# Kernel optimization log

Hardware: AMD Instinct MI355X
Metric: run time of the kernel (lower is better)

## Reference

```python
import jax, jax.numpy as jnp
from jax import lax
import numpy as np

B, C_IN, IMG = 32, 4, 224
FH = FW = IMG // 8  # 28: three stride-2 maxpools
NA = 4
SCORE_T, IOU_T, MAXP = 0.7, 0.3, 10
EPS = 1e-5


def conv2d(x, w, b, pad):
    y = lax.conv_general_dilated(x, w, (1, 1), [(pad, pad), (pad, pad)],
                                 dimension_numbers=('NCHW', 'OIHW', 'NCHW'))
    return y + b[None, :, None, None]


def bn_eval(x, g, b):
    # eval-mode BN with running_mean=0, running_var=1 (fresh model), eps=1e-5
    return x * (g / jnp.sqrt(1.0 + EPS))[None, :, None, None] + b[None, :, None, None]


def maxpool2(x):
    return lax.reduce_window(x, -jnp.inf, lax.max, (1, 1, 2, 2), (1, 1, 2, 2), 'VALID')


def make_anchors():
    ys = (jnp.arange(FH) + 0.5) / FH
    xs = (jnp.arange(FW) + 0.5) / FW
    cy, cx = jnp.meshgrid(ys, xs, indexing='ij')
    cxy = jnp.stack([cx, cy], -1)  # [H,W,2], matches loop order y,x then anchor
    sizes = jnp.array([[16., 16.], [32., 32.], [64., 64.], [128., 128.]], jnp.float32) / 224.0
    a = jnp.concatenate([jnp.broadcast_to(cxy[:, :, None, :], (FH, FW, NA, 2)),
                         jnp.broadcast_to(sizes[None, None], (FH, FW, NA, 2))], -1)
    return a.reshape(-1, 4)  # [H*W*NA, 4] = [3136, 4]


def decode_boxes(anchors, offsets):
    centers = anchors[..., :2] + offsets[..., :2] * 0.1
    sizes = anchors[..., 2:] * jnp.exp(offsets[..., 2:] * 0.2)
    boxes = jnp.concatenate([centers - sizes / 2, centers + sizes / 2], -1)
    return jnp.clip(boxes, 0.0, 1.0)


def nms_single(boxes, scores):
    # greedy NMS, fixed MAXP iterations (== max_proposals_per_image cap)
    N = scores.shape[0]
    s0 = jnp.where(scores > SCORE_T, scores, -jnp.inf)  # score-threshold filter
    areas = (boxes[:, 2] - boxes[:, 0]) * (boxes[:, 3] - boxes[:, 1])
    idx_all = jnp.arange(N)

    def body(s, _):
        i = jnp.argmax(s)
        ok = s[i] > -jnp.inf
        bi = boxes[i]
        xx1 = jnp.maximum(bi[0], boxes[:, 0]); yy1 = jnp.maximum(bi[1], boxes[:, 1])
        xx2 = jnp.minimum(bi[2], boxes[:, 2]); yy2 = jnp.minimum(bi[3], boxes[:, 3])
        inter = jnp.clip(xx2 - xx1, 0.0) * jnp.clip(yy2 - yy1, 0.0)
        iou = inter / (areas[i] + areas - inter)
        sup = (iou > IOU_T) | (idx_all == i)
        s_next = jnp.where(ok & sup, -jnp.inf, s)
        return s_next, (jnp.where(ok, i, 0), ok)

    _, (idxs, oks) = lax.scan(body, s0, None, length=MAXP)
    return idxs, oks  # [MAXP] int32, [MAXP] bool


def _forward(x, r1w, r1b, g1, b1, r2w, r2b, g2, b2, r3w, r3b, g3, b3, rpw, rpb,
             clsw, clsb, regw, regb, c1w, c1b, cg1, cb1, c2w, c2b, cg2, cb2,
             fc1w, fc1b, fc2w, fc2b, fc3w, fc3b, fc4w, fc4b):
    Bsz = x.shape[0]
    # --- Stage 1: lightweight RPN ---
    h = maxpool2(jax.nn.relu(bn_eval(conv2d(x, r1w, r1b, 1), g1, b1)))
    h = maxpool2(jax.nn.relu(bn_eval(conv2d(h, r2w, r2b, 1), g2, b2)))
    h = maxpool2(jax.nn.relu(bn_eval(conv2d(h, r3w, r3b, 1), g3, b3)))
    h = jax.nn.relu(conv2d(h, rpw, rpb, 1))
    cls = conv2d(h, clsw, clsb, 0).transpose(0, 2, 3, 1).reshape(Bsz, -1, 2)
    reg = conv2d(h, regw, regb, 0).transpose(0, 2, 3, 1).reshape(Bsz, -1, 4)
    anchors = make_anchors()
    probs = jax.nn.softmax(cls, -1)[..., 1]        # [B,N] objectness
    boxes = decode_boxes(anchors[None], reg)       # [B,N,4]
    # --- proposal selection: score threshold + greedy NMS + top-10 cap ---
    idxs, oks = jax.vmap(nms_single)(boxes, probs)  # [B,10]
    okf = oks.astype(boxes.dtype)
    kept_boxes = jax.vmap(lambda b, i: b[i])(boxes, idxs) * okf[..., None]
    kept_scores = jax.vmap(lambda s, i: s[i])(probs, idxs) * okf
    has_prop = (probs > SCORE_T).any(-1)           # [B]
    # --- Stage 2: CLM classifier (applied to the full image, as in original) ---
    f = jax.nn.relu(bn_eval(conv2d(x, c1w, c1b, 1), cg1, cb1))
    f = jax.nn.relu(bn_eval(conv2d(f, c2w, c2b, 1), cg2, cb2))
    # AdaptiveAvgPool2d((7,7)) on 224x224 -> mean over 32x32 blocks
    f = f.reshape(Bsz, 128, 7, 32, 7, 32).mean(axis=(3, 5)).reshape(Bsz, -1)
    f = jax.nn.relu(f @ fc1w + fc1b)
    f = jax.nn.relu(f @ fc2w + fc2b)
    f = jax.nn.relu(f @ fc3w + fc3b)
    logits = f @ fc4w + fc4b
    bg = jnp.array([1.0, 0.0], logits.dtype)
    final = jnp.where(has_prop[:, None], logits, bg[None])
    return final, kept_boxes, kept_scores, oks


def setup_inputs() -> dict:
    key = jax.random.key(0)
    ks = iter(jax.random.split(key, 64))

    def conv_w(o, i, k):
        return jax.random.normal(next(ks), (o, i, k, k), jnp.float32) * float(np.sqrt(2.0 / (i * k * k)))

    def lin_w(i, o):
        return jax.random.normal(next(ks), (i, o), jnp.float32) * float(1.0 / np.sqrt(i))

    return {
        'x': jax.random.normal(next(ks), (B, C_IN, IMG, IMG), jnp.float32),
        'r1w': conv_w(32, 4, 3), 'r1b': jnp.zeros(32), 'g1': jnp.ones(32), 'b1': jnp.zeros(32),
        'r2w': conv_w(64, 32, 3), 'r2b': jnp.zeros(64), 'g2': jnp.ones(64), 'b2': jnp.zeros(64),
        'r3w': conv_w(128, 64, 3), 'r3b': jnp.zeros(128), 'g3': jnp.ones(128), 'b3': jnp.zeros(128),
        'rpw': conv_w(256, 128, 3), 'rpb': jnp.zeros(256),
        'clsw': conv_w(8, 256, 1), 'clsb': jnp.zeros(8),
        'regw': conv_w(16, 256, 1), 'regb': jnp.zeros(16),
        'c1w': conv_w(64, 4, 3), 'c1b': jnp.zeros(64), 'cg1': jnp.ones(64), 'cb1': jnp.zeros(64),
        'c2w': conv_w(128, 64, 3), 'c2b': jnp.zeros(128), 'cg2': jnp.ones(128), 'cb2': jnp.zeros(128),
        'fc1w': lin_w(6272, 512), 'fc1b': jnp.zeros(512),
        'fc2w': lin_w(512, 256), 'fc2b': jnp.zeros(256),
        'fc3w': lin_w(256, 128), 'fc3b': jnp.zeros(128),
        'fc4w': lin_w(128, 2), 'fc4b': jnp.zeros(2),
    }


def reference(x, r1w, r1b, g1, b1, r2w, r2b, g2, b2, r3w, r3b, g3, b3, rpw, rpb,
              clsw, clsb, regw, regb, c1w, c1b, cg1, cb1, c2w, c2b, cg2, cb2,
              fc1w, fc1b, fc2w, fc2b, fc3w, fc3b, fc4w, fc4b):
    return _forward(x, r1w, r1b, g1, b1, r2w, r2b, g2, b2, r3w, r3b, g3, b3, rpw, rpb,
                    clsw, clsb, regw, regb, c1w, c1b, cg1, cb1, c2w, c2b, cg2, cb2,
                    fc1w, fc1b, fc2w, fc2b, fc3w, fc3b, fc4w, fc4b)
```

## Files before the change

### kernel.cpp

```cpp
#include <hip/hip_runtime.h>
#include <math.h>

constexpr int NANCH = 3136;
constexpr float SCORE_T = 0.7f;
constexpr float IOU_T = 0.3f;
constexpr int MAXP = 10;

typedef unsigned short u16;
typedef __attribute__((ext_vector_type(8))) short short8x;
typedef __attribute__((ext_vector_type(4))) float f32x4;

__device__ inline u16 f2bf(float f) {
  unsigned u = __builtin_bit_cast(unsigned, f);
  u += 0x7fffu + ((u >> 16) & 1u);
  return (u16)(u >> 16);
}
__device__ inline float bf2f(u16 h) {
  unsigned u = ((unsigned)h) << 16;
  return __builtin_bit_cast(float, u);
}

__global__ __launch_bounds__(256) void w1prep_k(const float* __restrict__ w,
                                                u16* __restrict__ hi, u16* __restrict__ lo,
                                                int COUT) {
  const int i = blockIdx.x * 256 + threadIdx.x;
  if (i >= COUT * 64) return;
  const int k = i & 63, co = i >> 6;
  float v = 0.f;
  if (k < 36) { const int tap = k >> 2, cin = k & 3; v = w[co * 36 + cin * 9 + tap]; }
  const u16 h = f2bf(v);
  hi[i] = h;
  lo[i] = f2bf(v - bf2f(h));
}

template<int MODE>
__global__ __launch_bounds__(256) void c1mfma_k(
    const float* __restrict__ x,
    const u16* __restrict__ wfh, const u16* __restrict__ wfl,
    const float* __restrict__ bias, const float* __restrict__ gamma,
    const float* __restrict__ beta,
    u16* __restrict__ outhi, u16* __restrict__ outlo) {
  constexpr int COUT = MODE ? 32 : 64;
  constexpr int NF   = MODE ? 2 : 4;
  constexpr int PS   = MODE ? 136 : 72;
  __shared__ u16 s_patch[64 * PS];
  __shared__ u16 s_wh[COUT * 72];
  __shared__ u16 s_wl[MODE ? COUT * 72 : 8];
  __shared__ float s_raw[4 * 6 * 18];
  __shared__ float s_pool[MODE ? 4 * 16 * 17 : 1];
  __shared__ u16 s_out[MODE ? 8 : 64 * 72];

  const int tid = threadIdx.x, lane = tid & 63, w = tid >> 6;
  const int lr = lane & 15, lg = lane >> 4;
  const int img = blockIdx.z;
  const int x0 = blockIdx.x * 16, y0 = blockIdx.y * 4;

  for (int i = tid; i < 64 * 7; i += 256) {
    const int p = i / 7, q = i % 7;
    *(uint2*)&s_patch[p * PS + 36 + q * 4] = make_uint2(0, 0);
    if (MODE) *(uint2*)&s_patch[p * PS + 100 + q * 4] = make_uint2(0, 0);
  }
  for (int i = tid; i < 432; i += 256) {
    const int cin = i / 108, r = i % 108;
    const int ry = r / 18, rx = r % 18;
    const int gy = y0 - 1 + ry, gx = x0 - 1 + rx;
    float v = 0.f;
    if ((unsigned)gy < 224u && (unsigned)gx < 224u)
      v = x[(((size_t)img * 4 + cin) * 224 + gy) * 224 + gx];
    s_raw[i] = v;
  }
  for (int i = tid; i < COUT * 8; i += 256) {
    const int co = i >> 3, q = i & 7;
    *(uint4*)&s_wh[co * 72 + q * 8] = *(const uint4*)&wfh[co * 64 + q * 8];
    if (MODE) *(uint4*)&s_wl[co * 72 + q * 8] = *(const uint4*)&wfl[co * 64 + q * 8];
  }
  __syncthreads();

  for (int i = tid; i < 576; i += 256) {
    const int p = i / 9, tap = i % 9;
    const int ty = p >> 4, tx = p & 15;
    const int ky = tap / 3, kx = tap % 3;
    u16 h4[4], l4[4];
#pragma unroll
    for (int cin = 0; cin < 4; cin++) {
      const float v = s_raw[cin * 108 + (ty + ky) * 18 + (tx + kx)];
      h4[cin] = f2bf(v);
      if (MODE) l4[cin] = f2bf(v - bf2f(h4[cin]));
    }
    *(uint2*)&s_patch[p * PS + tap * 4] = *(uint2*)h4;
    if (MODE) *(uint2*)&s_patch[p * PS + 64 + tap * 4] = *(uint2*)l4;
  }
  __syncthreads();

  int pA;
  if (MODE) pA = ((w >> 1) * 2 + (lr >> 3)) * 16 + (w & 1) * 8 + (lr & 7);
  else      pA = w * 16 + lr;

  f32x4 acc[NF];
#pragma unroll
  for (int nf = 0; nf < NF; nf++) acc[nf] = (f32x4)(0.f);

#pragma unroll
  for (int ks = 0; ks < 2; ks++) {
    const short8x ah = *(const short8x*)&s_patch[pA * PS + ks * 32 + lg * 8];
    short8x al;
    if (MODE) al = *(const short8x*)&s_patch[pA * PS + 64 + ks * 32 + lg * 8];
#pragma unroll
    for (int nf = 0; nf < NF; nf++) {
      const short8x bh = *(const short8x*)&s_wh[(nf * 16 + lr) * 72 + ks * 32 + lg * 8];
      if (MODE) {
        const short8x bl = *(const short8x*)&s_wl[(nf * 16 + lr) * 72 + ks * 32 + lg * 8];
        acc[nf] = __builtin_amdgcn_mfma_f32_16x16x32_bf16(al, bh, acc[nf], 0, 0, 0);
        acc[nf] = __builtin_amdgcn_mfma_f32_16x16x32_bf16(ah, bl, acc[nf], 0, 0, 0);
      }
      acc[nf] = __builtin_amdgcn_mfma_f32_16x16x32_bf16(ah, bh, acc[nf], 0, 0, 0);
    }
  }

  const float rsq = 1.f / sqrtf(1.f + 1e-5f);

  if (MODE == 0) {
#pragma unroll
    for (int nf = 0; nf < 4; nf++) {
      const int co = nf * 16 + lr;
      const float bi = bias[co], scl = gamma[co] * rsq, shf = beta[co];
#pragma unroll
      for (int j = 0; j < 4; j++) {
        const float e = fmaxf((acc[nf][j] + bi) * scl + shf, 0.f);
        s_out[(w * 16 + lg * 4 + j) * 72 + co] = f2bf(e);
      }
    }
    __syncthreads();
    for (int i = tid; i < 512; i += 256) {
      const int p = i >> 3, q = i & 7;
      const int oy = y0 + (p >> 4), ox = x0 + (p & 15);
      *(uint4*)&outhi[(((size_t)img * 224 + oy) * 224 + ox) * 64 + q * 8] =
          *(uint4*)&s_out[p * 72 + q * 8];
    }
  } else {
#pragma unroll
    for (int nf = 0; nf < 2; nf++) {
      const int co = nf * 16 + lr;
      const float bi = bias[co], scl = gamma[co] * rsq, shf = beta[co];
#pragma unroll
      for (int j = 0; j < 4; j++) {
        const int m = lg * 4 + j;
        s_pool[w * 272 + m * 17 + lr] = (acc[nf][j] + bi) * scl + shf;
      }
      __syncthreads();
      {
        const int pc = lane >> 4, n = lane & 15;
        const float* sp = &s_pool[w * 272];
        float m0 = fmaxf(sp[(pc * 2) * 17 + n], sp[(pc * 2 + 1) * 17 + n]);
        float m1 = fmaxf(sp[(pc * 2 + 8) * 17 + n], sp[(pc * 2 + 9) * 17 + n]);
        const float mm = fmaxf(fmaxf(m0, m1), 0.f);
        const int py = (y0 >> 1) + (w >> 1), px = (x0 >> 1) + (w & 1) * 4 + pc;
        const size_t o = (((size_t)img * 112 + py) * 112 + px) * 32 + nf * 16 + n;
        const u16 h = f2bf(mm);
        outhi[o] = h; outlo[o] = f2bf(mm - bf2f(h));
      }
      __syncthreads();
    }
  }
}

__global__ __launch_bounds__(256) void wsplit_k(const float* __restrict__ w,
                                                u16* __restrict__ hi, u16* __restrict__ lo,
                                                int COUT, int CIN) {
  const int n = 9 * COUT * CIN;
  const int i = blockIdx.x * 256 + threadIdx.x;
  if (i >= n) return;
  const int cin = i % CIN; int r = i / CIN;
  const int cout = r % COUT; const int tap = r / COUT;
  const float v = w[((size_t)cout * CIN + cin) * 9 + tap];
  const u16 h = f2bf(v);
  hi[i] = h; lo[i] = f2bf(v - bf2f(h));
}

__global__ __launch_bounds__(256) void w2b_k(const float* __restrict__ w,
                                             u16* __restrict__ wb) {
  const int i = blockIdx.x * 256 + threadIdx.x;
  if (i >= 73728) return;
  const int cin = i & 63; const int r = i >> 6;
  const int cout = r & 127; const int tap = r >> 7;
  wb[i] = f2bf(w[(((size_t)cout * 64 + cin) * 3 + tap / 3) * 3 + tap % 3]);
}

template<int CINCH, bool POOL, bool BN>
__global__ __launch_bounds__(256) void sconv_k(
    const u16* __restrict__ ahi, const u16* __restrict__ alo,
    const u16* __restrict__ whi, const u16* __restrict__ wlo,
    const float* __restrict__ bias, const float* __restrict__ gamma,
    const float* __restrict__ beta,
    u16* __restrict__ ohi, u16* __restrict__ olo, float* __restrict__ of32,
    int H, int W, int COUT, int cog) {
  __shared__ u16 s_in[6 * 34 * 72];
  __shared__ u16 s_w[64 * 72];
  const int tid = threadIdx.x, lane = tid & 63, wave = tid >> 6;
  const int wm = wave >> 1, wn = wave & 1, lr = lane & 15, lg = lane >> 4;
  const int img = blockIdx.z / cog, co0 = (blockIdx.z % cog) * 64;
  const int x0 = blockIdx.x * 32, band = blockIdx.y;
  const int CIN = CINCH * 32;

  f32x4 acc[4][2];
#pragma unroll
  for (int mi = 0; mi < 4; ++mi) { acc[mi][0] = (f32x4)(0.f); acc[mi][1] = (f32x4)(0.f); }

  for (int cc2 = 0; cc2 < CINCH; ++cc2) {
    for (int idx = tid; idx < 1632; idx += 256) {
      const int r = idx / 272, rem = idx % 272;
      const int c = rem >> 3, q = rem & 7, pl = q >> 2, qq = q & 3;
      const int gy = band * 4 - 1 + r, gx = x0 - 1 + c;
      uint4 v = make_uint4(0, 0, 0, 0);
      if ((unsigned)gy < (unsigned)H && (unsigned)gx < (unsigned)W) {
        const u16* src = pl ? alo : ahi;
        v = *(const uint4*)(src + ((size_t)(img * H + gy) * W + gx) * CIN + cc2 * 32 + qq * 8);
      }
      *(uint4*)(&s_in[(r * 34 + c) * 72 + pl * 32 + qq * 8]) = v;
    }
    for (int tap = 0; tap < 9; ++tap) {
      const int ky = tap / 3, kx = tap % 3;
      for (int idx = tid; idx < 512; idx += 256) {
        const int cout = idx >> 3, q = idx & 7, pl = q >> 2, qq = q & 3;
        const u16* src = pl ? wlo : whi;
        uint4 v = *(const uint4*)(src + ((size_t)tap * COUT + co0 + cout) * CIN + cc2 * 32 + qq * 8);
        *(uint4*)(&s_w[cout * 72 + pl * 32 + qq * 8]) = v;
      }
      __syncthreads();
      short8x ah[4], al[4], bh[2], bl[2];
#pragma unroll
      for (int mi = 0; mi < 4; ++mi) {
        const int base = ((2 * wm + (mi >> 1) + ky) * 34 + (mi & 1) * 16 + lr + kx) * 72;
        ah[mi] = *(const short8x*)(&s_in[base + lg * 8]);
        al[mi] = *(const short8x*)(&s_in[base + 32 + lg * 8]);
      }
#pragma unroll
      for (int ni = 0; ni < 2; ++ni) {
        const int wb2 = (wn * 32 + ni * 16 + lr) * 72;
        bh[ni] = *(const short8x*)(&s_w[wb2 + lg * 8]);
        bl[ni] = *(const short8x*)(&s_w[wb2 + 32 + lg * 8]);
      }
#pragma unroll
      for (int mi = 0; mi < 4; ++mi)
#pragma unroll
        for (int ni = 0; ni < 2; ++ni) {
          acc[mi][ni] = __builtin_amdgcn_mfma_f32_16x16x32_bf16(al[mi], bh[ni], acc[mi][ni], 0, 0, 0);
          acc[mi][ni] = __builtin_amdgcn_mfma_f32_16x16x32_bf16(ah[mi], bl[ni], acc[mi][ni], 0, 0, 0);
          acc[mi][ni] = __builtin_amdgcn_mfma_f32_16x16x32_bf16(ah[mi], bh[ni], acc[mi][ni], 0, 0, 0);
        }
      __syncthreads();
    }
  }

  const float rsq = 1.f / sqrtf(1.f + 1e-5f);
#pragma unroll
  for (int ni = 0; ni < 2; ++ni) {
    const int cout = co0 + wn * 32 + ni * 16 + lr;
    const float bi = bias[cout];
    const float scl = BN ? gamma[cout] * rsq : 1.f;
    const float shf = BN ? beta[cout] : 0.f;
    if (POOL) {
      const int OH = H >> 1, OW = W >> 1;
      const int py = band * 2 + wm;
#pragma unroll
      for (int ch = 0; ch < 2; ++ch)
#pragma unroll
        for (int jp = 0; jp < 2; ++jp) {
          float m = (acc[ch][ni][2 * jp] + bi) * scl + shf;
          m = fmaxf(m, (acc[ch][ni][2 * jp + 1] + bi) * scl + shf);
          m = fmaxf(m, (acc[ch + 2][ni][2 * jp] + bi) * scl + shf);
          m = fmaxf(m, (acc[ch + 2][ni][2 * jp + 1] + bi) * scl + shf);
          m = fmaxf(m, 0.f);
          const int px = (x0 >> 1) + ch * 8 + lg * 2 + jp;
          if (px < OW) {
            const size_t o = ((size_t)(img * OH + py) * OW + px) * COUT + cout;
            const u16 h = f2bf(m);
            ohi[o] = h; olo[o] = f2bf(m - bf2f(h));
          }
        }
    } else {
#pragma unroll
      for (int mi = 0; mi < 4; ++mi) {
        const int row = band * 4 + 2 * wm + (mi >> 1);
#pragma unroll
        for (int j = 0; j < 4; ++j) {
          const int px = x0 + (mi & 1) * 16 + lg * 4 + j;
          if (px < W)
            of32[((size_t)(img * H + row) * W + px) * COUT + cout] =
                fmaxf(acc[mi][ni][j] + bi, 0.f);
        }
      }
    }
  }
}

__global__ __launch_bounds__(256) void c2band_k(
    const u16* __restrict__ act, const u16* __restrict__ wb,
    const float* __restrict__ bias, const float* __restrict__ gamma,
    const float* __restrict__ beta, float* __restrict__ pooled, int gimg0) {
  __shared__ u16 s_in[6 * 34 * 72];
  __shared__ u16 s_w[2 * 128 * 40];
  __shared__ float s_pool[128];

  const int tid = threadIdx.x;
  const int lane = tid & 63, wave = tid >> 6;
  const int wm = wave >> 1, wn = wave & 1;
  const int lr = lane & 15, lg = lane >> 4;
  const int img = blockIdx.z >> 3, band = blockIdx.z & 7;
  const int x0 = blockIdx.x * 32, y0 = blockIdx.y * 32;
  const float rsq = 1.f / sqrtf(1.f + 1e-5f);

  if (tid < 128) s_pool[tid] = 0.f;

  for (int idx = tid; idx < 1632; idx += 256) {
    const int r = idx / 272, rem = idx % 272;
    const int c = rem >> 3, q = rem & 7;
    const int gy = y0 + band * 4 - 1 + r, gx = x0 - 1 + c;
    uint4 v = make_uint4(0, 0, 0, 0);
    if ((unsigned)gy < 224u && (unsigned)gx < 224u)
      v = *(const uint4*)(act + (((size_t)img * 224 + gy) * 224 + gx) * 64 + q * 8);
    *(uint4*)(&s_in[(r * 34 + c) * 72 + q * 8]) = v;
  }

  f32x4 acc[4][4];
#pragma unroll
  for (int mi = 0; mi < 4; ++mi)
#pragma unroll
    for (int ni = 0; ni < 4; ++ni) acc[mi][ni] = (f32x4)(0.f);

  for (int tap = 0; tap < 9; ++tap) {
    const int ky = tap / 3, kx = tap % 3;
    for (int idx = tid; idx < 1024; idx += 256) {
      const int cout = idx >> 3, q = idx & 7;
      uint4 v = *(const uint4*)(wb + ((size_t)tap * 128 + cout) * 64 + q * 8);
      *(uint4*)(&s_w[(q >> 2) * 5120 + cout * 40 + (q & 3) * 8]) = v;
    }
    __syncthreads();
#pragma unroll
    for (int h = 0; h < 2; ++h) {
      short8x a[4], bf[4];
#pragma unroll
      for (int mi = 0; mi < 4; ++mi) {
        const int rl = wm * 2 + (mi >> 1) + ky;
        const int cc = (mi & 1) * 16 + lr + kx;
        a[mi] = *(const short8x*)(&s_in[(rl * 34 + cc) * 72 + h * 32 + lg * 8]);
      }
#pragma unroll
      for (int ni = 0; ni < 4; ++ni) {
        const int co = wn * 64 + ni * 16 + lr;
        bf[ni] = *(const short8x*)(&s_w[h * 5120 + co * 40 + lg * 8]);
      }
#pragma unroll
      for (int mi = 0; mi < 4; ++mi)
#pragma unroll
        for (int ni = 0; ni < 4; ++ni)
          acc[mi][ni] = __builtin_amdgcn_mfma_f32_16x16x32_bf16(a[mi], bf[ni], acc[mi][ni], 0, 0, 0);
    }
    __syncthreads();
  }
#pragma unroll
  for (int ni = 0; ni < 4; ++ni) {
    const int co = wn * 64 + ni * 16 + lr;
    const float bi = bias[co], scl = gamma[co] * rsq, shf = beta[co];
    float s = 0.f;
#pragma unroll
    for (int mi = 0; mi < 4; ++mi)
#pragma unroll
      for (int j = 0; j < 4; ++j)
        s += fmaxf((acc[mi][ni][j] + bi) * scl + shf, 0.f);
    atomicAdd(&s_pool[co], s);
  }
  __syncthreads();
  if (tid < 128)
    atomicAdd(&pooled[(size_t)(gimg0 + img) * 6272 + tid * 49 + blockIdx.y * 7 + blockIdx.x],
              s_pool[tid] * (1.f / 1024.f));
}

__global__ __launch_bounds__(256) void rpn_head_k(
    const float* __restrict__ feat,
    const float* __restrict__ clsw, const float* __restrict__ clsb,
    const float* __restrict__ regw, const float* __restrict__ regb,
    float* __restrict__ probs, float* __restrict__ boxes) {
  const int gid = blockIdx.x * 256 + threadIdx.x;
  if (gid >= 32 * NANCH) return;
  const int a = gid & 3;
  int r = gid >> 2;
  const int x = r % 28; r /= 28;
  const int y = r % 28;
  const int b = r / 28;

  const float* f = feat + ((size_t)b * 784 + y * 28 + x) * 256;
  float c0 = clsb[2 * a], c1 = clsb[2 * a + 1];
  float r0 = regb[4 * a], r1 = regb[4 * a + 1], r2 = regb[4 * a + 2], r3 = regb[4 * a + 3];
#pragma unroll 4
  for (int c = 0; c < 256; c++) {
    const float fv = f[c];
    c0 = fmaf(fv, clsw[(2 * a) * 256 + c], c0);
    c1 = fmaf(fv, clsw[(2 * a + 1) * 256 + c], c1);
    r0 = fmaf(fv, regw[(4 * a) * 256 + c], r0);
    r1 = fmaf(fv, regw[(4 * a + 1) * 256 + c], r1);
    r2 = fmaf(fv, regw[(4 * a + 2) * 256 + c], r2);
    r3 = fmaf(fv, regw[(4 * a + 3) * 256 + c], r3);
  }
  const float p = 1.f / (1.f + expf(c0 - c1));

  const float cx = (x + 0.5f) * (1.f / 28.f);
  const float cy = (y + 0.5f) * (1.f / 28.f);
  const float sz = (float)(16 << a) * (1.f / 224.f);
  const float ncx = cx + r0 * 0.1f, ncy = cy + r1 * 0.1f;
  const float nw = sz * expf(r2 * 0.2f), nh = sz * expf(r3 * 0.2f);
  const float x1 = fminf(fmaxf(ncx - nw * 0.5f, 0.f), 1.f);
  const float y1 = fminf(fmaxf(ncy - nh * 0.5f, 0.f), 1.f);
  const float x2 = fminf(fmaxf(ncx + nw * 0.5f, 0.f), 1.f);
  const float y2 = fminf(fmaxf(ncy + nh * 0.5f, 0.f), 1.f);

  probs[gid] = p;
  ((float4*)boxes)[gid] = make_float4(x1, y1, x2, y2);
}

__global__ __launch_bounds__(256) void nms_k(
    const float* __restrict__ probs, const float* __restrict__ boxes,
    float* __restrict__ dout, int* __restrict__ hasflag) {
  const int b = blockIdx.x;
  const int t = threadIdx.x;
  __shared__ float sc[NANCH];
  __shared__ float ar[NANCH];
  __shared__ float4 bx[NANCH];
  __shared__ float rv[256];
  __shared__ int   ri[256];
  __shared__ int s_any, s_sel[MAXP], s_ok[MAXP];

  if (t == 0) s_any = 0;
  __syncthreads();

  int anyl = 0;
  for (int i = t; i < NANCH; i += 256) {
    const float p = probs[(size_t)b * NANCH + i];
    const float4 bb = ((const float4*)boxes)[(size_t)b * NANCH + i];
    bx[i] = bb;
    ar[i] = (bb.z - bb.x) * (bb.w - bb.y);
    sc[i] = (p > SCORE_T) ? p : -INFINITY;
    if (p > SCORE_T) anyl = 1;
  }
  if (anyl) atomicOr(&s_any, 1);
  __syncthreads();

  for (int it = 0; it < MAXP; ++it) {
    float bv = -INFINITY; int bi = 0x7fffffff;
    for (int i = t; i < NANCH; i += 256) {
      const float v = sc[i];
      if (v > bv || (v == bv && i < bi)) { bv = v; bi = i; }
    }
    rv[t] = bv; ri[t] = bi;
    __syncthreads();
    for (int st = 128; st > 0; st >>= 1) {
      if (t < st) {
        const float ov = rv[t + st]; const int oi = ri[t + st];
        if (ov > rv[t] || (ov == rv[t] && oi < ri[t])) { rv[t] = ov; ri[t] = oi; }
      }
      __syncthreads();
    }
    if (t == 0) { s_sel[it] = ri[0]; s_ok[it] = (rv[0] > -INFINITY) ? 1 : 0; }
    __syncthreads();
    const int sel = s_sel[it];
    const int ok  = s_ok[it];
    if (ok) {
      const float4 bs = bx[sel]; const float as = ar[sel];
      for (int i = t; i < NANCH; i += 256) {
        const float xx1 = fmaxf(bs.x, bx[i].x), yy1 = fmaxf(bs.y, bx[i].y);
        const float xx2 = fminf(bs.z, bx[i].z), yy2 = fminf(bs.w, bx[i].w);
        const float inter = fmaxf(xx2 - xx1, 0.f) * fmaxf(yy2 - yy1, 0.f);
        const float iou = inter / (as + ar[i] - inter);
        if (iou > IOU_T || i == sel) sc[i] = -INFINITY;
      }
    }
    __syncthreads();
  }

  if (t < MAXP) {
    const int sel = s_ok[t] ? s_sel[t] : 0;
    const float okf = s_ok[t] ? 1.f : 0.f;
    const float4 bb = bx[sel];
    float* kb = dout + 64;
    float* ks = dout + 64 + 32 * MAXP * 4;
    float* ko = dout + 64 + 32 * MAXP * 5;
    const size_t base = ((size_t)b * MAXP + t) * 4;
    kb[base + 0] = bb.x * okf; kb[base + 1] = bb.y * okf;
    kb[base + 2] = bb.z * okf; kb[base + 3] = bb.w * okf;
    ks[b * MAXP + t] = probs[(size_t)b * NANCH + sel] * okf;
    ko[b * MAXP + t] = okf;
  }
  if (t == 0) hasflag[b] = s_any;
}

__global__ __launch_bounds__(64) void fcsplit_k(
    const float* __restrict__ x, const float* __restrict__ w,
    float* __restrict__ part, int K, int N, int kchunk) {
  extern __shared__ float sx[];
  const int o = blockIdx.x * 64 + threadIdx.x;
  const int k0 = blockIdx.y * kchunk;
  for (int i = threadIdx.x; i < 32 * kchunk; i += 64) {
    const int bb = i / kchunk, kk = i % kchunk;
    sx[i] = x[(size_t)bb * K + k0 + kk];
  }
  __syncthreads();
  float acc[32];
#pragma unroll
  for (int bb = 0; bb < 32; bb++) acc[bb] = 0.f;
#pragma unroll 8
  for (int kk = 0; kk < kchunk; kk++) {
    const float wv = w[(size_t)(k0 + kk) * N + o];
#pragma unroll
    for (int bb = 0; bb < 32; bb++) acc[bb] = fmaf(sx[bb * kchunk + kk], wv, acc[bb]);
  }
  float* p = part + (size_t)blockIdx.y * 32 * N + o;
#pragma unroll
  for (int bb = 0; bb < 32; bb++) p[(size_t)bb * N] = acc[bb];
}

__global__ __launch_bounds__(256) void fcreduce_k(
    const float* __restrict__ part, const float* __restrict__ bias,
    float* __restrict__ y, int N, int KT, int dorelu) {
  const int i = blockIdx.x * 256 + threadIdx.x;
  if (i >= 32 * N) return;
  const int o = i % N;
  float s = bias[o];
  for (int kt = 0; kt < KT; kt++) s += part[(size_t)kt * 32 * N + i];
  y[i] = dorelu ? fmaxf(s, 0.f) : s;
}

__global__ __launch_bounds__(64) void final_k(
    const float* __restrict__ f3, const float* __restrict__ w,
    const float* __restrict__ bi, const int* __restrict__ hasflag,
    float* __restrict__ dout) {
  const int t = threadIdx.x;
  if (t >= 64) return;
  const int b = t >> 1, j = t & 1;
  float acc = bi[j];
#pragma unroll 4
  for (int k = 0; k < 128; k++) acc = fmaf(f3[b * 128 + k], w[k * 2 + j], acc);
  dout[b * 2 + j] = hasflag[b] ? acc : (j == 0 ? 1.f : 0.f);
}

extern "C" void kernel_launch(void* const* d_in, const int* in_sizes, int n_in,
                              void* d_out, int out_size, void* d_ws, size_t ws_size,
                              hipStream_t stream) {
  const float* x    = (const float*)d_in[0];
  const float* r1w  = (const float*)d_in[1];  const float* r1b = (const float*)d_in[2];
  const float* g1   = (const float*)d_in[3];  const float* b1  = (const float*)d_in[4];
  const float* r2w  = (const float*)d_in[5];  const float* r2b = (const float*)d_in[6];
  const float* g2   = (const float*)d_in[7];  const float* b2  = (const float*)d_in[8];
  const float* r3w  = (const float*)d_in[9];  const float* r3b = (const float*)d_in[10];
  const float* g3   = (const float*)d_in[11]; const float* b3  = (const float*)d_in[12];
  const float* rpw  = (const float*)d_in[13]; const float* rpb = (const float*)d_in[14];
  const float* clsw = (const float*)d_in[15]; const float* clsb = (const float*)d_in[16];
  const float* regw = (const float*)d_in[17]; const float* regb = (const float*)d_in[18];
  const float* c1w  = (const float*)d_in[19]; const float* c1b = (const float*)d_in[20];
  const float* cg1  = (const float*)d_in[21]; const float* cb1 = (const float*)d_in[22];
  const float* c2w  = (const float*)d_in[23]; const float* c2b = (const float*)d_in[24];
  const float* cg2  = (const float*)d_in[25]; const float* cb2 = (const float*)d_in[26];
  const float* fc1w = (const float*)d_in[27]; const float* fc1b = (const float*)d_in[28];
  const float* fc2w = (const float*)d_in[29]; const float* fc2b = (const float*)d_in[30];
  const float* fc3w = (const float*)d_in[31]; const float* fc3b = (const float*)d_in[32];
  const float* fc4w = (const float*)d_in[33]; const float* fc4b = (const float*)d_in[34];
  float* dout = (float*)d_out;
  float* Wp = (float*)d_ws;

  const size_t o_h1   = 0;
  const size_t o_h2   = 12845056;
  const size_t o_h3   = o_h2 + 6422528;
  const size_t o_prob = o_h3 + 3211264;
  const size_t o_box  = o_prob + 100352;
  const size_t o_flag = o_box + 401408;
  const size_t o_pool = o_flag + 32;
  const size_t o_f1   = o_pool + 200704;
  const size_t o_f2   = o_f1 + 16384;
  const size_t o_f3   = o_f2 + 8192;
  const size_t o_w2b  = o_f3 + 4096;
  const size_t o_w2s  = o_w2b + 36864;
  const size_t o_w3s  = o_w2s + 18432;
  const size_t o_wps  = o_w3s + 73728;
  const size_t o_w1r  = o_wps + 294912;
  const size_t o_w1c  = o_w1r + 2048;

  u16* h1hi = (u16*)(Wp + o_h1); u16* h1lo = h1hi + 12845056;
  u16* h2hi = (u16*)(Wp + o_h2); u16* h2lo = h2hi + 6422528;
  u16* h3hi = (u16*)(Wp + o_h3); u16* h3lo = h3hi + 3211264;
  float* probs = Wp + o_prob; float* boxes = Wp + o_box;
  int* hasflag = (int*)(Wp + o_flag);
  float* pooled = Wp + o_pool;
  float* f1 = Wp + o_f1; float* f2 = Wp + o_f2; float* f3 = Wp + o_f3;
  u16* w2b  = (u16*)(Wp + o_w2b);
  u16* w2hi = (u16*)(Wp + o_w2s); u16* w2lo = w2hi + 18432;
  u16* w3hi = (u16*)(Wp + o_w3s); u16* w3lo = w3hi + 73728;
  u16* wphi = (u16*)(Wp + o_wps); u16* wplo = wphi + 294912;
  u16* w1rhi = (u16*)(Wp + o_w1r); u16* w1rlo = w1rhi + 2048;
  u16* w1chi = (u16*)(Wp + o_w1c); u16* w1clo = w1chi + 4096;
  float* h4f32 = Wp + o_h1;
  u16*   c1buf = (u16*)(Wp + o_h1);
  float* fcpart = Wp + o_h1;

  wsplit_k<<<(9 * 64 * 32 + 255) / 256, 256, 0, stream>>>(r2w, w2hi, w2lo, 64, 32);
  wsplit_k<<<(9 * 128 * 64 + 255) / 256, 256, 0, stream>>>(r3w, w3hi, w3lo, 128, 64);
  wsplit_k<<<(9 * 256 * 128 + 255) / 256, 256, 0, stream>>>(rpw, wphi, wplo, 256, 128);
  w2b_k<<<288, 256, 0, stream>>>(c2w, w2b);
  w1prep_k<<<8, 256, 0, stream>>>(r1w, w1rhi, w1rlo, 32);
  w1prep_k<<<16, 256, 0, stream>>>(c1w, w1chi, w1clo, 64);

  c1mfma_k<1><<<dim3(14, 56, 32), 256, 0, stream>>>(
      x, w1rhi, w1rlo, r1b, g1, b1, h1hi, h1lo);
  sconv_k<1, true, true><<<dim3(4, 28, 32), 256, 0, stream>>>(
      h1hi, h1lo, w2hi, w2lo, r2b, g2, b2, h2hi, h2lo, nullptr, 112, 112, 64, 1);
  sconv_k<2, true, true><<<dim3(2, 14, 64), 256, 0, stream>>>(
      h2hi, h2lo, w3hi, w3lo, r3b, g3, b3, h3hi, h3lo, nullptr, 56, 56, 128, 2);
  sconv_k<4, false, false><<<dim3(1, 7, 128), 256, 0, stream>>>(
      h3hi, h3lo, wphi, wplo, rpb, rpb, rpb, nullptr, nullptr, h4f32, 28, 28, 256, 4);

  rpn_head_k<<<(32 * NANCH + 255) / 256, 256, 0, stream>>>(h4f32, clsw, clsb, regw, regb, probs, boxes);
  nms_k<<<32, 256, 0, stream>>>(probs, boxes, dout, hasflag);

  hipMemsetAsync(pooled, 0, 32 * 6272 * sizeof(float), stream);
  constexpr int CHUNK = 8;
  for (int c0 = 0; c0 < 32; c0 += CHUNK) {
    c1mfma_k<0><<<dim3(14, 56, CHUNK), 256, 0, stream>>>(
        x + (size_t)c0 * 4 * 224 * 224, w1chi, w1clo, c1b, cg1, cb1, c1buf, nullptr);
    c2band_k<<<dim3(7, 7, CHUNK * 8), 256, 0, stream>>>(
        c1buf, w2b, c2b, cg2, cb2, pooled, c0);
  }

  fcsplit_k<<<dim3(8, 64), 64, 32 * 98 * 4, stream>>>(pooled, fc1w, fcpart, 6272, 512, 98);
  fcreduce_k<<<64, 256, 0, stream>>>(fcpart, fc1b, f1, 512, 64, 1);
  fcsplit_k<<<dim3(4, 16), 64, 32 * 32 * 4, stream>>>(f1, fc2w, fcpart, 512, 256, 32);
  fcreduce_k<<<32, 256, 0, stream>>>(fcpart, fc2b, f2, 256, 16, 1);
  fcsplit_k<<<dim3(2, 8), 64, 32 * 32 * 4, stream>>>(f2, fc3w, fcpart, 256, 128, 32);
  fcreduce_k<<<16, 256, 0, stream>>>(fcpart, fc3b, f3, 128, 8, 1);
  final_k<<<1, 64, 0, stream>>>(f3, fc4w, fc4b, hasflag, dout);
}
```

Baseline: 1.162 ms.

## Load conv2 weights directly into registers and reduce pooling with shuffles

The classifier conv2 kernel no longer stages the per-tap weight tile through shared memory. Each lane reads its B fragments straight from global memory, which removes two barriers per tap and shrinks LDS use, and a launch bound hint asks for three blocks per SM. The pooled channel sums are now reduced with cross-lane shuffles and a small per-wave shared array instead of shared-memory atomics. The cost is redundant global weight loads across waves and blocks, which rely on cache hits, plus higher register pressure from the unrolled tap loop.

```diff
diff --git a/kernel.cpp b/kernel.cpp
--- a/kernel.cpp
+++ b/kernel.cpp
@@ -294,13 +294,12 @@
   }
 }
 
-__global__ __launch_bounds__(256) void c2band_k(
+__global__ __launch_bounds__(256, 3) void c2band_k(
     const u16* __restrict__ act, const u16* __restrict__ wb,
     const float* __restrict__ bias, const float* __restrict__ gamma,
     const float* __restrict__ beta, float* __restrict__ pooled, int gimg0) {
   __shared__ u16 s_in[6 * 34 * 72];
-  __shared__ u16 s_w[2 * 128 * 40];
-  __shared__ float s_pool[128];
+  __shared__ float s_wp[256];
 
   const int tid = threadIdx.x;
   const int lane = tid & 63, wave = tid >> 6;
@@ -309,8 +308,6 @@
   const int img = blockIdx.z >> 3, band = blockIdx.z & 7;
   const int x0 = blockIdx.x * 32, y0 = blockIdx.y * 32;
   const float rsq = 1.f / sqrtf(1.f + 1e-5f);
-
-  if (tid < 128) s_pool[tid] = 0.f;
 
   for (int idx = tid; idx < 1632; idx += 256) {
     const int r = idx / 272, rem = idx % 272;
@@ -321,6 +318,7 @@
       v = *(const uint4*)(act + (((size_t)img * 224 + gy) * 224 + gx) * 64 + q * 8);
     *(uint4*)(&s_in[(r * 34 + c) * 72 + q * 8]) = v;
   }
+  __syncthreads();
 
   f32x4 acc[4][4];
 #pragma unroll
@@ -328,17 +326,20 @@
 #pragma unroll
     for (int ni = 0; ni < 4; ++ni) acc[mi][ni] = (f32x4)(0.f);
 
+  const u16* wbase = wb + ((size_t)(wn * 64 + lr)) * 64 + lg * 8;
+
+#pragma unroll
   for (int tap = 0; tap < 9; ++tap) {
     const int ky = tap / 3, kx = tap % 3;
-    for (int idx = tid; idx < 1024; idx += 256) {
-      const int cout = idx >> 3, q = idx & 7;
-      uint4 v = *(const uint4*)(wb + ((size_t)tap * 128 + cout) * 64 + q * 8);
-      *(uint4*)(&s_w[(q >> 2) * 5120 + cout * 40 + (q & 3) * 8]) = v;
-    }
-    __syncthreads();
+    short8x bfr[2][4];
+#pragma unroll
+    for (int h = 0; h < 2; ++h)
+#pragma unroll
+      for (int ni = 0; ni < 4; ++ni)
+        bfr[h][ni] = *(const short8x*)(wbase + tap * 8192 + ni * 1024 + h * 32);
 #pragma unroll
     for (int h = 0; h < 2; ++h) {
-      short8x a[4], bf[4];
+      short8x a[4];
 #pragma unroll
       for (int mi = 0; mi < 4; ++mi) {
         const int rl = wm * 2 + (mi >> 1) + ky;
@@ -346,18 +347,14 @@
         a[mi] = *(const short8x*)(&s_in[(rl * 34 + cc) * 72 + h * 32 + lg * 8]);
       }
 #pragma unroll
-      for (int ni = 0; ni < 4; ++ni) {
-        const int co = wn * 64 + ni * 16 + lr;
-        bf[ni] = *(const short8x*)(&s_w[h * 5120 + co * 40 + lg * 8]);
-      }
-#pragma unroll
       for (int mi = 0; mi < 4; ++mi)
 #pragma unroll
         for (int ni = 0; ni < 4; ++ni)
-          acc[mi][ni] = __builtin_amdgcn_mfma_f32_16x16x32_bf16(a[mi], bf[ni], acc[mi][ni], 0, 0, 0);
-    }
-    __syncthreads();
-  }
+          acc[mi][ni] = __builtin_amdgcn_mfma_f32_16x16x32_bf16(a[mi], bfr[h][ni], acc[mi][ni], 0, 0, 0);
+    }
+  }
+
+  float part[4];
 #pragma unroll
   for (int ni = 0; ni < 4; ++ni) {
     const int co = wn * 64 + ni * 16 + lr;
@@ -368,12 +365,22 @@
 #pragma unroll
       for (int j = 0; j < 4; ++j)
         s += fmaxf((acc[mi][ni][j] + bi) * scl + shf, 0.f);
-    atomicAdd(&s_pool[co], s);
+    s += __shfl_xor(s, 16);
+    s += __shfl_xor(s, 32);
+    part[ni] = s;
+  }
+  if (lane < 16) {
+#pragma unroll
+    for (int ni = 0; ni < 4; ++ni)
+      s_wp[wave * 64 + ni * 16 + lr] = part[ni];
   }
   __syncthreads();
-  if (tid < 128)
+  if (tid < 128) {
+    const int w0 = tid >> 6, idx = tid & 63;
+    const float v = s_wp[w0 * 64 + idx] + s_wp[(w0 + 2) * 64 + idx];
     atomicAdd(&pooled[(size_t)(gimg0 + img) * 6272 + tid * 49 + blockIdx.y * 7 + blockIdx.x],
-              s_pool[tid] * (1.f / 1024.f));
+              v * (1.f / 1024.f));
+  }
 }
 
 __global__ __launch_bounds__(256) void rpn_head_k(
```

Result: slower. 1.371 ms (+18.0%).
